# Kernel optimization log

Measured on AMD Instinct MI355X. Metric: run time of the kernel, lower is better.

The kernel has to match this reference:

```python
import jax, jax.numpy as jnp
import numpy as np

NUM_PPR_NODES = 262144
BATCH = 4096
K = NUM_PPR_NODES // BATCH  # ppr neighbors per batch node
F_IN, H, C = 256, 512, 64


def setup_inputs() -> dict:
    key = jax.random.key(0)
    ks = jax.random.split(key, 6)
    X = jax.random.normal(ks[0], (NUM_PPR_NODES, F_IN), dtype=jnp.float32)
    ppr_scores = jax.random.uniform(ks[1], (NUM_PPR_NODES,), dtype=jnp.float32)
    # sorted batch ids; last element == BATCH-1 so dim_size = ppr_idx[-1]+1 = BATCH
    ppr_idx = jnp.repeat(jnp.arange(BATCH, dtype=jnp.int64), K)
    s1 = 1.0 / np.sqrt(F_IN)
    s2 = 1.0 / np.sqrt(H)
    Wa = jax.random.uniform(ks[2], (F_IN, H), jnp.float32, -s1, s1)
    Wb = jax.random.uniform(ks[3], (H, H), jnp.float32, -s2, s2)
    Wc = jax.random.uniform(ks[4], (H, H), jnp.float32, -s2, s2)
    Wd = jax.random.uniform(ks[5], (H, C), jnp.float32, -s2, s2)
    return {"X": X, "ppr_scores": ppr_scores, "ppr_idx": ppr_idx,
            "Wa": Wa, "Wb": Wb, "Wc": Wc, "Wd": Wd}


def reference(X, ppr_scores, ppr_idx, Wa, Wb, Wc, Wd):
    # embedding MLP (dropout inactive at eval): Linear -> ReLU -> Linear, no bias
    emb = jax.nn.relu(X @ Wa) @ Wb                      # [N, H]
    # weighted scatter-sum over ppr neighborhoods
    weighted = emb * ppr_scores[:, None]                # [N, H]
    agg = jax.ops.segment_sum(weighted, ppr_idx, num_segments=BATCH)  # [B, H]
    # logit MLP: Linear -> ReLU -> Linear, no bias
    logits = jax.nn.relu(agg @ Wc) @ Wd                 # [B, C]
    return logits
```

## Files before the change

### kernel.cpp

```cpp
#include <hip/hip_runtime.h>

typedef short bs8 __attribute__((ext_vector_type(8)));
typedef float fx4 __attribute__((ext_vector_type(4)));

__device__ __forceinline__ unsigned short f2bf(float f) {
    unsigned u = __builtin_bit_cast(unsigned, f);
    u += 0x7FFFu + ((u >> 16) & 1u);
    return (unsigned short)(u >> 16);
}

__device__ __forceinline__ bs8 load_cvt8(const float* p) {
    fx4 u = *(const fx4*)p;
    fx4 v = *(const fx4*)(p + 4);
    bs8 r;
    r[0] = (short)f2bf(u[0]); r[1] = (short)f2bf(u[1]);
    r[2] = (short)f2bf(u[2]); r[3] = (short)f2bf(u[3]);
    r[4] = (short)f2bf(v[0]); r[5] = (short)f2bf(v[1]);
    r[6] = (short)f2bf(v[2]); r[7] = (short)f2bf(v[3]);
    return r;
}

__global__ void pack_b(const float* __restrict__ src, unsigned short* __restrict__ dst,
                       int KN, int N) {
    const int l = threadIdx.x;
    const int lr = l & 15, lg = l >> 4;
    const int bid = blockIdx.x;
    const int cf = bid / KN, kc = bid % KN;
    const int col  = cf * 16 + lr;
    const int krow = kc * 32 + lg * 8;
    const size_t ob = ((size_t)bid * 64 + l) * 8;
    #pragma unroll
    for (int j = 0; j < 8; ++j)
        dst[ob + j] = f2bf(src[(size_t)(krow + j) * N + col]);
}

__global__ __launch_bounds__(256) void wbc_gemm(const float* __restrict__ Wb,
                                                const float* __restrict__ Wc,
                                                float* __restrict__ Wbc) {
    __shared__ float As[32][33];
    __shared__ float Bs[32][33];
    const int tx = threadIdx.x & 15, ty = threadIdx.x >> 4;
    const int i0 = blockIdx.y * 32, j0 = blockIdx.x * 32;
    float c00 = 0.f, c01 = 0.f, c10 = 0.f, c11 = 0.f;
    for (int k0 = 0; k0 < 512; k0 += 32) {
        for (int t = threadIdx.x; t < 1024; t += 256) {
            int r = t >> 5, c = t & 31;
            As[r][c] = Wb[(size_t)(i0 + r) * 512 + k0 + c];
            Bs[r][c] = Wc[(size_t)(k0 + r) * 512 + j0 + c];
        }
        __syncthreads();
        #pragma unroll
        for (int k = 0; k < 32; ++k) {
            float a0 = As[ty * 2][k], a1 = As[ty * 2 + 1][k];
            float b0 = Bs[k][tx * 2], b1 = Bs[k][tx * 2 + 1];
            c00 += a0 * b0; c01 += a0 * b1; c10 += a1 * b0; c11 += a1 * b1;
        }
        __syncthreads();
    }
    Wbc[(size_t)(i0 + ty * 2) * 512 + j0 + tx * 2]         = c00;
    Wbc[(size_t)(i0 + ty * 2) * 512 + j0 + tx * 2 + 1]     = c01;
    Wbc[(size_t)(i0 + ty * 2 + 1) * 512 + j0 + tx * 2]     = c10;
    Wbc[(size_t)(i0 + ty * 2 + 1) * 512 + j0 + tx * 2 + 1] = c11;
}

__global__ __launch_bounds__(256, 2) void k1_fused(
    const float* __restrict__ X, const float* __restrict__ scores,
    const bs8* __restrict__ WaP, unsigned short* __restrict__ aggH) {
    const int tid = threadIdx.x;
    const int w = tid >> 6, l = tid & 63;
    const int lr = l & 15, lg = l >> 4;
    const int seg = blockIdx.x * 4 + w;
    const size_t row0 = (size_t)seg * 64;

    bs8 a[4][8];
    {
        const float* xb = X + (row0 + lr) * 256 + lg * 8;
        #pragma unroll
        for (int mf = 0; mf < 4; ++mf)
            #pragma unroll
            for (int kc = 0; kc < 8; ++kc)
                a[mf][kc] = load_cvt8(xb + mf * (16 * 256) + kc * 32);
    }
    float sc[4][4];
    #pragma unroll
    for (int mf = 0; mf < 4; ++mf) {
        fx4 s = *(const fx4*)(scores + row0 + mf * 16 + lg * 4);
        sc[mf][0] = s[0]; sc[mf][1] = s[1]; sc[mf][2] = s[2]; sc[mf][3] = s[3];
    }

    #pragma unroll 1
    for (int cc = 0; cc < 8; ++cc) {
        fx4 acc[4][4];
        #pragma unroll
        for (int mf = 0; mf < 4; ++mf)
            #pragma unroll
            for (int nf = 0; nf < 4; ++nf)
                acc[mf][nf] = (fx4){0.f, 0.f, 0.f, 0.f};

        #pragma unroll
        for (int kc = 0; kc < 8; ++kc) {
            bs8 b[4];
            #pragma unroll
            for (int nf = 0; nf < 4; ++nf)
                b[nf] = WaP[((cc * 4 + nf) * 8 + kc) * 64 + l];
            #pragma unroll
            for (int mf = 0; mf < 4; ++mf)
                #pragma unroll
                for (int nf = 0; nf < 4; ++nf)
                    acc[mf][nf] = __builtin_amdgcn_mfma_f32_16x16x32_bf16(
                        a[mf][kc], b[nf], acc[mf][nf], 0, 0, 0);
        }
        #pragma unroll
        for (int nf = 0; nf < 4; ++nf) {
            float p = 0.f;
            #pragma unroll
            for (int mf = 0; mf < 4; ++mf)
                #pragma unroll
                for (int r = 0; r < 4; ++r) {
                    float v = acc[mf][nf][r];
                    v = v > 0.f ? v : 0.f;
                    p += v * sc[mf][r];
                }
            p += __shfl_xor(p, 16, 64);
            p += __shfl_xor(p, 32, 64);
            if (lg == 0)
                aggH[(size_t)seg * 512 + cc * 64 + nf * 16 + lr] = f2bf(p);
        }
    }
}

__global__ __launch_bounds__(256) void k2_gemm(
    const unsigned short* __restrict__ aggH, const bs8* __restrict__ WbcP,
    unsigned short* __restrict__ T) {
    const int tid = threadIdx.x;
    const int w = tid >> 6, l = tid & 63, lr = l & 15, lg = l >> 4;
    const int gw = blockIdx.x * 4 + w;
    const int rg = gw >> 3, cg = gw & 7;
    const int r0 = rg * 64, c0 = cg * 64;

    fx4 acc[4][4];
    #pragma unroll
    for (int mf = 0; mf < 4; ++mf)
        #pragma unroll
        for (int nf = 0; nf < 4; ++nf)
            acc[mf][nf] = (fx4){0.f, 0.f, 0.f, 0.f};

    #pragma unroll 1
    for (int kc = 0; kc < 16; ++kc) {
        bs8 a[4], b[4];
        #pragma unroll
        for (int mf = 0; mf < 4; ++mf)
            a[mf] = *(const bs8*)(aggH + (size_t)(r0 + mf * 16 + lr) * 512 + kc * 32 + lg * 8);
        #pragma unroll
        for (int nf = 0; nf < 4; ++nf)
            b[nf] = WbcP[((cg * 4 + nf) * 16 + kc) * 64 + l];
        #pragma unroll
        for (int mf = 0; mf < 4; ++mf)
            #pragma unroll
            for (int nf = 0; nf < 4; ++nf)
                acc[mf][nf] = __builtin_amdgcn_mfma_f32_16x16x32_bf16(
                    a[mf], b[nf], acc[mf][nf], 0, 0, 0);
    }
    #pragma unroll
    for (int mf = 0; mf < 4; ++mf)
        #pragma unroll
        for (int nf = 0; nf < 4; ++nf)
            #pragma unroll
            for (int r = 0; r < 4; ++r) {
                float v = fmaxf(acc[mf][nf][r], 0.f);
                T[(size_t)(r0 + mf * 16 + lg * 4 + r) * 512 + c0 + nf * 16 + lr] = f2bf(v);
            }
}

__global__ __launch_bounds__(256) void k3_gemm(
    const unsigned short* __restrict__ T, const bs8* __restrict__ WdP,
    float* __restrict__ out) {
    const int tid = threadIdx.x;
    const int w = tid >> 6, l = tid & 63, lr = l & 15, lg = l >> 4;
    const int gw = blockIdx.x * 4 + w;
    const int r0 = gw * 64;

    fx4 acc[4][4];
    #pragma unroll
    for (int mf = 0; mf < 4; ++mf)
        #pragma unroll
        for (int nf = 0; nf < 4; ++nf)
            acc[mf][nf] = (fx4){0.f, 0.f, 0.f, 0.f};

    #pragma unroll 1
    for (int kc = 0; kc < 16; ++kc) {
        bs8 a[4], b[4];
        #pragma unroll
        for (int mf = 0; mf < 4; ++mf)
            a[mf] = *(const bs8*)(T + (size_t)(r0 + mf * 16 + lr) * 512 + kc * 32 + lg * 8);
        #pragma unroll
        for (int nf = 0; nf < 4; ++nf)
            b[nf] = WdP[(nf * 16 + kc) * 64 + l];
        #pragma unroll
        for (int mf = 0; mf < 4; ++mf)
            #pragma unroll
            for (int nf = 0; nf < 4; ++nf)
                acc[mf][nf] = __builtin_amdgcn_mfma_f32_16x16x32_bf16(
                    a[mf], b[nf], acc[mf][nf], 0, 0, 0);
    }
    #pragma unroll
    for (int mf = 0; mf < 4; ++mf)
        #pragma unroll
        for (int nf = 0; nf < 4; ++nf)
            #pragma unroll
            for (int r = 0; r < 4; ++r)
                out[(size_t)(r0 + mf * 16 + lg * 4 + r) * 64 + nf * 16 + lr] = acc[mf][nf][r];
}

extern "C" void kernel_launch(void* const* d_in, const int* in_sizes, int n_in,
                              void* d_out, int out_size, void* d_ws, size_t ws_size,
                              hipStream_t stream) {
    const float* X  = (const float*)d_in[0];
    const float* sc = (const float*)d_in[1];
    const float* Wa = (const float*)d_in[3];
    const float* Wb = (const float*)d_in[4];
    const float* Wc = (const float*)d_in[5];
    const float* Wd = (const float*)d_in[6];
    float* out = (float*)d_out;

    char* ws = (char*)d_ws;
    unsigned short* WaP  = (unsigned short*)(ws + 0);
    unsigned short* WbcP = (unsigned short*)(ws + 262144);
    unsigned short* WdP  = (unsigned short*)(ws + 786432);
    float*          Wbc  = (float*)         (ws + 851968);
    unsigned short* aggH = (unsigned short*)(ws + 1900544);
    unsigned short* T    = (unsigned short*)(ws + 6094848);

    pack_b<<<dim3(32 * 8),  dim3(64), 0, stream>>>(Wa,  WaP,  8,  512);
    wbc_gemm<<<dim3(16, 16), dim3(256), 0, stream>>>(Wb, Wc, Wbc);
    pack_b<<<dim3(32 * 16), dim3(64), 0, stream>>>(Wbc, WbcP, 16, 512);
    pack_b<<<dim3(4 * 16),  dim3(64), 0, stream>>>(Wd,  WdP,  16, 64);

    k1_fused<<<dim3(1024), dim3(256), 0, stream>>>(X, sc, (const bs8*)WaP, aggH);
    k2_gemm<<<dim3(128),   dim3(256), 0, stream>>>(aggH, (const bs8*)WbcP, T);
    k3_gemm<<<dim3(16),    dim3(256), 0, stream>>>(T, (const bs8*)WdP, out);
}
```

Measured before the change: 197.9 us.

## Split each segment across four waves sharing an LDS-staged bf16 X tile

Each block now handles one 64-row segment instead of four. The X tile is converted to bf16 and staged once in swizzled shared memory, and each wave computes two of the eight 64-column chunks of the hidden layer. This cuts per-wave register pressure (the old code held 32 bs8 A fragments per wave) and quadruples the grid, which should raise parallelism and occupancy. In exchange it adds a 32KB LDS footprint per block, a block-wide barrier, and LDS reads inside the inner loop.

New measurement: 189.5 us. 1.04x faster.

```diff
diff --git a/kernel.cpp b/kernel.cpp
--- a/kernel.cpp
+++ b/kernel.cpp
@@ -66,30 +66,29 @@
 __global__ __launch_bounds__(256, 2) void k1_fused(
     const float* __restrict__ X, const float* __restrict__ scores,
     const bs8* __restrict__ WaP, unsigned short* __restrict__ aggH) {
+    __shared__ unsigned short xt[64 * 256];
+
     const int tid = threadIdx.x;
+    const int seg = blockIdx.x;
+    const size_t row0 = (size_t)seg * 64;
+
+    #pragma unroll
+    for (int it = 0; it < 8; ++it) {
+        const int flat = it * 2048 + tid * 8;
+        const int r = flat >> 8, c = flat & 255;
+        bs8 v = load_cvt8(X + (row0 + r) * 256 + c);
+        int byte = r * 512 + c * 2;
+        byte ^= (r & 7) << 4;
+        *(bs8*)((char*)xt + byte) = v;
+    }
+    __syncthreads();
+
     const int w = tid >> 6, l = tid & 63;
     const int lr = l & 15, lg = l >> 4;
-    const int seg = blockIdx.x * 4 + w;
-    const size_t row0 = (size_t)seg * 64;
-
-    bs8 a[4][8];
-    {
-        const float* xb = X + (row0 + lr) * 256 + lg * 8;
-        #pragma unroll
-        for (int mf = 0; mf < 4; ++mf)
-            #pragma unroll
-            for (int kc = 0; kc < 8; ++kc)
-                a[mf][kc] = load_cvt8(xb + mf * (16 * 256) + kc * 32);
-    }
-    float sc[4][4];
-    #pragma unroll
-    for (int mf = 0; mf < 4; ++mf) {
-        fx4 s = *(const fx4*)(scores + row0 + mf * 16 + lg * 4);
-        sc[mf][0] = s[0]; sc[mf][1] = s[1]; sc[mf][2] = s[2]; sc[mf][3] = s[3];
-    }
 
     #pragma unroll 1
-    for (int cc = 0; cc < 8; ++cc) {
+    for (int ci = 0; ci < 2; ++ci) {
+        const int cc = w * 2 + ci;
         fx4 acc[4][4];
         #pragma unroll
         for (int mf = 0; mf < 4; ++mf)
@@ -103,12 +102,27 @@
             #pragma unroll
             for (int nf = 0; nf < 4; ++nf)
                 b[nf] = WaP[((cc * 4 + nf) * 8 + kc) * 64 + l];
+            bs8 a[4];
+            #pragma unroll
+            for (int mf = 0; mf < 4; ++mf) {
+                const int row = mf * 16 + lr;
+                int byte = row * 512 + kc * 64 + lg * 16;
+                byte ^= (row & 7) << 4;
+                a[mf] = *(const bs8*)((const char*)xt + byte);
+            }
             #pragma unroll
             for (int mf = 0; mf < 4; ++mf)
                 #pragma unroll
                 for (int nf = 0; nf < 4; ++nf)
                     acc[mf][nf] = __builtin_amdgcn_mfma_f32_16x16x32_bf16(
-                        a[mf][kc], b[nf], acc[mf][nf], 0, 0, 0);
+                        a[mf], b[nf], acc[mf][nf], 0, 0, 0);
+        }
+
+        float sc0[4][4];
+        #pragma unroll
+        for (int mf = 0; mf < 4; ++mf) {
+            fx4 s = *(const fx4*)(scores + row0 + mf * 16 + lg * 4);
+            sc0[mf][0] = s[0]; sc0[mf][1] = s[1]; sc0[mf][2] = s[2]; sc0[mf][3] = s[3];
         }
         #pragma unroll
         for (int nf = 0; nf < 4; ++nf) {
@@ -119,7 +133,7 @@
                 for (int r = 0; r < 4; ++r) {
                     float v = acc[mf][nf][r];
                     v = v > 0.f ? v : 0.f;
-                    p += v * sc[mf][r];
+                    p += v * sc0[mf][r];
                 }
             p += __shfl_xor(p, 16, 64);
             p += __shfl_xor(p, 32, 64);
@@ -236,7 +250,7 @@
     pack_b<<<dim3(32 * 16), dim3(64), 0, stream>>>(Wbc, WbcP, 16, 512);
     pack_b<<<dim3(4 * 16),  dim3(64), 0, stream>>>(Wd,  WdP,  16, 64);
 
-    k1_fused<<<dim3(1024), dim3(256), 0, stream>>>(X, sc, (const bs8*)WaP, aggH);
+    k1_fused<<<dim3(4096), dim3(256), 0, stream>>>(X, sc, (const bs8*)WaP, aggH);
     k2_gemm<<<dim3(128),   dim3(256), 0, stream>>>(aggH, (const bs8*)WbcP, T);
     k3_gemm<<<dim3(16),    dim3(256), 0, stream>>>(T, (const bs8*)WdP, out);
 }
```
